# Kernel optimization log

Measured on AMD Instinct MI355X. Metric: run time of the kernel, lower is better.

Reference implementation:

```python
import jax, jax.numpy as jnp
import numpy as np

N_TOTAL = 524288  # total entity embeddings in flat ragged buffer
A = 262144        # number of actors
D = 256           # d_model
C = 32            # n_choice


def setup_inputs() -> dict:
    key = jax.random.key(0)
    k1, k2, k3, k4, k5 = jax.random.split(key, 5)
    x_data = jax.random.normal(k1, (N_TOTAL, D), dtype=jnp.float32)
    W = jax.random.normal(k2, (C, D), dtype=jnp.float32) * 0.01  # layer_init std=0.01
    b = jnp.zeros((C,), dtype=jnp.float32)
    actors = jax.random.randint(k3, (A,), 0, N_TOTAL, dtype=jnp.int64)
    mask = jax.random.randint(k4, (A, C), 0, 2, dtype=jnp.int32)
    mask = mask.at[:, 0].set(1)  # guarantee at least one valid choice per actor
    pa = jax.random.randint(k5, (A,), 0, C, dtype=jnp.int64)
    # prev_actions must be valid under the mask (as a real rollout would be)
    valid = jnp.take_along_axis(mask, pa[:, None], axis=1).squeeze(-1)
    prev_actions = jnp.where(valid != 0, pa, 0)
    return {"x_data": x_data, "W": W, "b": b, "actors": actors,
            "mask": mask, "prev_actions": prev_actions}


def reference(x_data, W, b, actors, mask, prev_actions):
    # gather actor embeddings: [A, D]
    actor_embeds = x_data[actors]
    # linear projection: [A, C]
    logits = jnp.einsum('ad,cd->ac', actor_embeds, W) + b
    # masked fill with -inf where mask == 0
    logits = jnp.where(mask == 0, -jnp.inf, logits)
    # Categorical: normalized logits = log_softmax
    logp = jax.nn.log_softmax(logits, axis=-1)
    p = jnp.exp(logp)
    action = prev_actions  # prev_actions provided -> no sampling
    logprob = jnp.take_along_axis(logp, action[:, None], axis=1).squeeze(-1)
    # entropy: -sum p*logp over valid entries (0*(-inf) -> 0)
    entropy = -jnp.sum(jnp.where(mask != 0, p * logp, 0.0), axis=-1)
    return action, logprob, entropy, logp
```

## Files before the change

### kernel.cpp

```cpp
#include <hip/hip_runtime.h>
#include <math.h>


constexpr int A_TOTAL = 262144;
constexpr int DMODEL  = 256;
constexpr int NCHOICE = 32;
constexpr int BATCH   = 32;
constexpr int PADC    = 36;

#define MASK_NEG 1.0e30f

#define DPP_SUM_STEP(x, ctrl)                                              \
    (x) += __int_as_float(__builtin_amdgcn_update_dpp(                     \
        0, __float_as_int(x), (ctrl), 0xf, 0xf, true))
#define DPP_MAX_STEP(x, ctrl)                                              \
    (x) = fmaxf((x), __int_as_float(__builtin_amdgcn_update_dpp(           \
        0, __float_as_int(x), (ctrl), 0xf, 0xf, true)))

#define DPP_REDUCE_DG(x)                                                   \
    do { DPP_SUM_STEP(x, 0xB1); DPP_SUM_STEP(x, 0x4E);                     \
         DPP_SUM_STEP(x, 0x128); DPP_SUM_STEP(x, 0x124); } while (0)

#define DPP_RED8_SUM(x)                                                    \
    do { DPP_SUM_STEP(x, 0xB1); DPP_SUM_STEP(x, 0x4E);                     \
         DPP_SUM_STEP(x, 0x141); } while (0)
#define DPP_RED8_MAX(x)                                                    \
    do { DPP_MAX_STEP(x, 0xB1); DPP_MAX_STEP(x, 0x4E);                     \
         DPP_MAX_STEP(x, 0x141); } while (0)

__global__ __launch_bounds__(256, 2)
void cat_action_head(const float* __restrict__ x_data,
                     const float* __restrict__ W,
                     const float* __restrict__ bvec,
                     const int*   __restrict__ actors,
                     const int*   __restrict__ mask,
                     const int*   __restrict__ prev_actions,
                     float* __restrict__ out)
{
    const int t  = threadIdx.x;
    const int wv = t >> 6;
    const int ln = t & 63;
    const int dg = ln & 15;
    const int cg = ln >> 4;

    float* out_action  = out;
    float* out_logprob = out + A_TOTAL;
    float* out_entropy = out + 2 * A_TOTAL;
    float* out_logp    = out + 3 * A_TOTAL;

    __shared__ float xs[BATCH][DMODEL];
    __shared__ float part[BATCH][PADC];

    const int abase = blockIdx.x * BATCH;

    const int aa  = t >> 3;
    const int q   = t & 7;
    const int aep = abase + aa;
    const int4   mv  = *reinterpret_cast<const int4*>(
                           &mask[(size_t)aep * NCHOICE + q * 4]);
    const float4 bq  = *reinterpret_cast<const float4*>(&bvec[q * 4]);
    const int    act = prev_actions[aep];

    {
        int acts[8];
#pragma unroll
        for (int j = 0; j < 8; ++j)
            acts[j] = actors[abase + wv * 8 + j];
#pragma unroll
        for (int j = 0; j < 8; ++j) {
            const float* src = x_data + (size_t)acts[j] * DMODEL + ln * 4;
            __builtin_amdgcn_global_load_lds(
                (const __attribute__((address_space(1))) void*)src,
                (__attribute__((address_space(3))) void*)&xs[wv * 8 + j][0],
                16, 0, 0);
        }
    }

    float4 Wf[8][4];
#pragma unroll
    for (int k = 0; k < 8; ++k) {
        const float* Wr = W + (size_t)(cg * 8 + k) * DMODEL + dg * 4;
#pragma unroll
        for (int j = 0; j < 4; ++j)
            Wf[k][j] = *reinterpret_cast<const float4*>(Wr + j * 64);
    }

    asm volatile("s_waitcnt vmcnt(0)" ::: "memory");

#pragma unroll 1
    for (int ii = 0; ii < 8; ++ii) {
        const int i = wv * 8 + ii;
        const float* xrow = &xs[i][dg * 4];
        float4 xv[4];
#pragma unroll
        for (int j = 0; j < 4; ++j)
            xv[j] = *reinterpret_cast<const float4*>(xrow + j * 64);

        float acc[8] = {0.f, 0.f, 0.f, 0.f, 0.f, 0.f, 0.f, 0.f};
#pragma unroll
        for (int j = 0; j < 4; ++j) {
#pragma unroll
            for (int k = 0; k < 8; ++k) {
                acc[k] = fmaf(xv[j].x, Wf[k][j].x, acc[k]);
                acc[k] = fmaf(xv[j].y, Wf[k][j].y, acc[k]);
                acc[k] = fmaf(xv[j].z, Wf[k][j].z, acc[k]);
                acc[k] = fmaf(xv[j].w, Wf[k][j].w, acc[k]);
            }
        }
#pragma unroll
        for (int k = 0; k < 8; ++k) DPP_REDUCE_DG(acc[k]);

        if (dg == 0) {
            float4 v0; v0.x = acc[0]; v0.y = acc[1]; v0.z = acc[2]; v0.w = acc[3];
            float4 v1; v1.x = acc[4]; v1.y = acc[5]; v1.z = acc[6]; v1.w = acc[7];
            *reinterpret_cast<float4*>(&part[i][cg * 8])     = v0;
            *reinterpret_cast<float4*>(&part[i][cg * 8 + 4]) = v1;
        }
    }

    {
        const float4 pv = *reinterpret_cast<const float4*>(&part[aa][q * 4]);

        const float lg0 = mv.x ? pv.x + bq.x : -MASK_NEG;
        const float lg1 = mv.y ? pv.y + bq.y : -MASK_NEG;
        const float lg2 = mv.z ? pv.z + bq.z : -MASK_NEG;
        const float lg3 = mv.w ? pv.w + bq.w : -MASK_NEG;

        float mx = fmaxf(fmaxf(lg0, lg1), fmaxf(lg2, lg3));
        DPP_RED8_MAX(mx);

        const float e0 = expf(lg0 - mx);
        const float e1 = expf(lg1 - mx);
        const float e2 = expf(lg2 - mx);
        const float e3 = expf(lg3 - mx);
        float se = (e0 + e1) + (e2 + e3);
        DPP_RED8_SUM(se);

        const float lse = mx + logf(se);
        const float rse = 1.0f / se;

        const float lp0 = lg0 - lse;
        const float lp1 = lg1 - lse;
        const float lp2 = lg2 - lse;
        const float lp3 = lg3 - lse;

        float4 lpv; lpv.x = lp0; lpv.y = lp1; lpv.z = lp2; lpv.w = lp3;
        *reinterpret_cast<float4*>(
            &out_logp[(size_t)aep * NCHOICE + q * 4]) = lpv;

        float ent = fmaf(e0, lp0, fmaf(e1, lp1, fmaf(e2, lp2, e3 * lp3)));
        DPP_RED8_SUM(ent);

        float sel = (act == q * 4 + 0) ? lp0 : 0.0f;
        sel = (act == q * 4 + 1) ? lp1 : sel;
        sel = (act == q * 4 + 2) ? lp2 : sel;
        sel = (act == q * 4 + 3) ? lp3 : sel;
        DPP_RED8_SUM(sel);

        if (q == 0) {
            out_logprob[aep] = sel;
            out_entropy[aep] = -ent * rse;
            out_action[aep]  = (float)act;
        }
    }
}

extern "C" void kernel_launch(void* const* d_in, const int* in_sizes, int n_in,
                              void* d_out, int out_size, void* d_ws, size_t ws_size,
                              hipStream_t stream)
{
    const float* x_data = (const float*)d_in[0];
    const float* W      = (const float*)d_in[1];
    const float* bvec   = (const float*)d_in[2];
    const int*   actors = (const int*)d_in[3];
    const int*   mask   = (const int*)d_in[4];
    const int*   prev   = (const int*)d_in[5];
    float*       o      = (float*)d_out;

    const int nblocks = A_TOTAL / BATCH;
    cat_action_head<<<nblocks, 256, 0, stream>>>(x_data, W, bvec, actors, mask,
                                                 prev, o);
}
```

Before: 107.1 us.

## Process 64 actors per block with double-buffered LDS gather pipeline

Each block now handles 64 actors, and each wave processes 16 of them in two chunks of 8. The gather into LDS for the second chunk is issued before computing the first, with a partial vmcnt wait so the gather overlaps the GEMV. Actor indices are loaded as int4 vectors, and LDS reads of the next row are software-prefetched during compute. In exchange, the W register load is amortized over twice as many actors, but there are half as many blocks and more LDS per block, which may reduce occupancy and latency hiding.

```diff
diff --git a/kernel.cpp b/kernel.cpp
--- a/kernel.cpp
+++ b/kernel.cpp
@@ -5,7 +5,7 @@
 constexpr int A_TOTAL = 262144;
 constexpr int DMODEL  = 256;
 constexpr int NCHOICE = 32;
-constexpr int BATCH   = 32;
+constexpr int APB     = 64;
 constexpr int PADC    = 36;
 
 #define MASK_NEG 1.0e30f
@@ -20,7 +20,6 @@
 #define DPP_REDUCE_DG(x)                                                   \
     do { DPP_SUM_STEP(x, 0xB1); DPP_SUM_STEP(x, 0x4E);                     \
          DPP_SUM_STEP(x, 0x128); DPP_SUM_STEP(x, 0x124); } while (0)
-
 #define DPP_RED8_SUM(x)                                                    \
     do { DPP_SUM_STEP(x, 0xB1); DPP_SUM_STEP(x, 0x4E);                     \
          DPP_SUM_STEP(x, 0x141); } while (0)
@@ -48,33 +47,49 @@
     float* out_entropy = out + 2 * A_TOTAL;
     float* out_logp    = out + 3 * A_TOTAL;
 
-    __shared__ float xs[BATCH][DMODEL];
-    __shared__ float part[BATCH][PADC];
-
-    const int abase = blockIdx.x * BATCH;
-
-    const int aa  = t >> 3;
-    const int q   = t & 7;
-    const int aep = abase + aa;
-    const int4   mv  = *reinterpret_cast<const int4*>(
-                           &mask[(size_t)aep * NCHOICE + q * 4]);
+    __shared__ float xs[4][2][8][DMODEL];
+    __shared__ float part[APB][PADC];
+
+    const int bbase = blockIdx.x * APB;
+    const int wb    = bbase + wv * 16;
+
+    const int q  = ln & 7;
+    const int p0 = wv * 16 + (ln >> 3);
+    const int p1 = p0 + 8;
+    const int a0 = bbase + p0;
+    const int a1 = bbase + p1;
+    const int4   mv0 = *reinterpret_cast<const int4*>(&mask[(size_t)a0 * NCHOICE + q * 4]);
+    const int4   mv1 = *reinterpret_cast<const int4*>(&mask[(size_t)a1 * NCHOICE + q * 4]);
     const float4 bq  = *reinterpret_cast<const float4*>(&bvec[q * 4]);
-    const int    act = prev_actions[aep];
-
+    const int    act0 = prev_actions[a0];
+    const int    act1 = prev_actions[a1];
+
+    int acts[16];
     {
-        int acts[8];
-#pragma unroll
-        for (int j = 0; j < 8; ++j)
-            acts[j] = actors[abase + wv * 8 + j];
-#pragma unroll
-        for (int j = 0; j < 8; ++j) {
-            const float* src = x_data + (size_t)acts[j] * DMODEL + ln * 4;
-            __builtin_amdgcn_global_load_lds(
-                (const __attribute__((address_space(1))) void*)src,
-                (__attribute__((address_space(3))) void*)&xs[wv * 8 + j][0],
-                16, 0, 0);
-        }
+        const int4 v0 = *reinterpret_cast<const int4*>(&actors[wb]);
+        const int4 v1 = *reinterpret_cast<const int4*>(&actors[wb + 4]);
+        const int4 v2 = *reinterpret_cast<const int4*>(&actors[wb + 8]);
+        const int4 v3 = *reinterpret_cast<const int4*>(&actors[wb + 12]);
+        acts[0]=v0.x; acts[1]=v0.y; acts[2]=v0.z; acts[3]=v0.w;
+        acts[4]=v1.x; acts[5]=v1.y; acts[6]=v1.z; acts[7]=v1.w;
+        acts[8]=v2.x; acts[9]=v2.y; acts[10]=v2.z; acts[11]=v2.w;
+        acts[12]=v3.x; acts[13]=v3.y; acts[14]=v3.z; acts[15]=v3.w;
     }
+
+#define STAGE(BUF, C)                                                       \
+    do {                                                                    \
+        _Pragma("unroll")                                                   \
+        for (int j = 0; j < 8; ++j) {                                       \
+            const float* src = x_data + (size_t)acts[(C) * 8 + j] * DMODEL  \
+                             + ln * 4;                                      \
+            __builtin_amdgcn_global_load_lds(                               \
+                (const __attribute__((address_space(1))) void*)src,         \
+                (__attribute__((address_space(3))) void*)&xs[wv][BUF][j][0],\
+                16, 0, 0);                                                  \
+        }                                                                   \
+    } while (0)
+
+    STAGE(0, 0);
 
     float4 Wf[8][4];
 #pragma unroll
@@ -85,84 +100,104 @@
             Wf[k][j] = *reinterpret_cast<const float4*>(Wr + j * 64);
     }
 
+    STAGE(1, 1);
+
+#define LDR(DST, BUF, II)                                                   \
+    do {                                                                    \
+        const float* xrow_ = &xs[wv][BUF][II][dg * 4];                      \
+        _Pragma("unroll")                                                   \
+        for (int j = 0; j < 4; ++j)                                         \
+            DST[j] = *reinterpret_cast<const float4*>(xrow_ + j * 64);      \
+    } while (0)
+
+#define COMPUTE(XV, C, II)                                                  \
+    do {                                                                    \
+        float acc[8] = {0.f,0.f,0.f,0.f,0.f,0.f,0.f,0.f};                   \
+        _Pragma("unroll")                                                   \
+        for (int j = 0; j < 4; ++j) {                                       \
+            _Pragma("unroll")                                               \
+            for (int k = 0; k < 8; ++k) {                                   \
+                acc[k] = fmaf(XV[j].x, Wf[k][j].x, acc[k]);                 \
+                acc[k] = fmaf(XV[j].y, Wf[k][j].y, acc[k]);                 \
+                acc[k] = fmaf(XV[j].z, Wf[k][j].z, acc[k]);                 \
+                acc[k] = fmaf(XV[j].w, Wf[k][j].w, acc[k]);                 \
+            }                                                               \
+        }                                                                   \
+        _Pragma("unroll")                                                   \
+        for (int k = 0; k < 8; ++k) DPP_REDUCE_DG(acc[k]);                  \
+        if (dg == 0) {                                                      \
+            const int p_ = wv * 16 + (C) * 8 + (II);                        \
+            float4 v0_; v0_.x=acc[0]; v0_.y=acc[1]; v0_.z=acc[2]; v0_.w=acc[3]; \
+            float4 v1_; v1_.x=acc[4]; v1_.y=acc[5]; v1_.z=acc[6]; v1_.w=acc[7]; \
+            *reinterpret_cast<float4*>(&part[p_][cg * 8])     = v0_;        \
+            *reinterpret_cast<float4*>(&part[p_][cg * 8 + 4]) = v1_;        \
+        }                                                                   \
+    } while (0)
+
+#define GEMV_CHUNK(C)                                                       \
+    do {                                                                    \
+        float4 xva[4], xvb[4];                                              \
+        LDR(xva, (C) & 1, 0);                                               \
+        _Pragma("unroll")                                                   \
+        for (int ii = 0; ii < 8; ii += 2) {                                 \
+            if (ii + 1 < 8) LDR(xvb, (C) & 1, ii + 1);                      \
+            COMPUTE(xva, C, ii);                                            \
+            if (ii + 2 < 8) LDR(xva, (C) & 1, ii + 2);                      \
+            COMPUTE(xvb, C, ii + 1);                                        \
+        }                                                                   \
+    } while (0)
+
+    asm volatile("s_waitcnt vmcnt(8)" ::: "memory");
+    GEMV_CHUNK(0);
     asm volatile("s_waitcnt vmcnt(0)" ::: "memory");
-
-#pragma unroll 1
-    for (int ii = 0; ii < 8; ++ii) {
-        const int i = wv * 8 + ii;
-        const float* xrow = &xs[i][dg * 4];
-        float4 xv[4];
-#pragma unroll
-        for (int j = 0; j < 4; ++j)
-            xv[j] = *reinterpret_cast<const float4*>(xrow + j * 64);
-
-        float acc[8] = {0.f, 0.f, 0.f, 0.f, 0.f, 0.f, 0.f, 0.f};
-#pragma unroll
-        for (int j = 0; j < 4; ++j) {
-#pragma unroll
-            for (int k = 0; k < 8; ++k) {
-                acc[k] = fmaf(xv[j].x, Wf[k][j].x, acc[k]);
-                acc[k] = fmaf(xv[j].y, Wf[k][j].y, acc[k]);
-                acc[k] = fmaf(xv[j].z, Wf[k][j].z, acc[k]);
-                acc[k] = fmaf(xv[j].w, Wf[k][j].w, acc[k]);
-            }
-        }
-#pragma unroll
-        for (int k = 0; k < 8; ++k) DPP_REDUCE_DG(acc[k]);
-
-        if (dg == 0) {
-            float4 v0; v0.x = acc[0]; v0.y = acc[1]; v0.z = acc[2]; v0.w = acc[3];
-            float4 v1; v1.x = acc[4]; v1.y = acc[5]; v1.z = acc[6]; v1.w = acc[7];
-            *reinterpret_cast<float4*>(&part[i][cg * 8])     = v0;
-            *reinterpret_cast<float4*>(&part[i][cg * 8 + 4]) = v1;
-        }
-    }
-
-    {
-        const float4 pv = *reinterpret_cast<const float4*>(&part[aa][q * 4]);
-
-        const float lg0 = mv.x ? pv.x + bq.x : -MASK_NEG;
-        const float lg1 = mv.y ? pv.y + bq.y : -MASK_NEG;
-        const float lg2 = mv.z ? pv.z + bq.z : -MASK_NEG;
-        const float lg3 = mv.w ? pv.w + bq.w : -MASK_NEG;
-
-        float mx = fmaxf(fmaxf(lg0, lg1), fmaxf(lg2, lg3));
-        DPP_RED8_MAX(mx);
-
-        const float e0 = expf(lg0 - mx);
-        const float e1 = expf(lg1 - mx);
-        const float e2 = expf(lg2 - mx);
-        const float e3 = expf(lg3 - mx);
-        float se = (e0 + e1) + (e2 + e3);
-        DPP_RED8_SUM(se);
-
-        const float lse = mx + logf(se);
-        const float rse = 1.0f / se;
-
-        const float lp0 = lg0 - lse;
-        const float lp1 = lg1 - lse;
-        const float lp2 = lg2 - lse;
-        const float lp3 = lg3 - lse;
-
-        float4 lpv; lpv.x = lp0; lpv.y = lp1; lpv.z = lp2; lpv.w = lp3;
-        *reinterpret_cast<float4*>(
-            &out_logp[(size_t)aep * NCHOICE + q * 4]) = lpv;
-
-        float ent = fmaf(e0, lp0, fmaf(e1, lp1, fmaf(e2, lp2, e3 * lp3)));
-        DPP_RED8_SUM(ent);
-
-        float sel = (act == q * 4 + 0) ? lp0 : 0.0f;
-        sel = (act == q * 4 + 1) ? lp1 : sel;
-        sel = (act == q * 4 + 2) ? lp2 : sel;
-        sel = (act == q * 4 + 3) ? lp3 : sel;
-        DPP_RED8_SUM(sel);
-
-        if (q == 0) {
-            out_logprob[aep] = sel;
-            out_entropy[aep] = -ent * rse;
-            out_action[aep]  = (float)act;
-        }
-    }
+    GEMV_CHUNK(1);
+
+#define EPILOGUE(PROW, AEP, MV, ACT)                                        \
+    do {                                                                    \
+        const float4 pv = *reinterpret_cast<const float4*>(&part[PROW][q * 4]); \
+        const float lg0 = (MV).x ? pv.x + bq.x : -MASK_NEG;                 \
+        const float lg1 = (MV).y ? pv.y + bq.y : -MASK_NEG;                 \
+        const float lg2 = (MV).z ? pv.z + bq.z : -MASK_NEG;                 \
+        const float lg3 = (MV).w ? pv.w + bq.w : -MASK_NEG;                 \
+        float mx = fmaxf(fmaxf(lg0, lg1), fmaxf(lg2, lg3));                 \
+        DPP_RED8_MAX(mx);                                                   \
+        const float e0 = expf(lg0 - mx);                                    \
+        const float e1 = expf(lg1 - mx);                                    \
+        const float e2 = expf(lg2 - mx);                                    \
+        const float e3 = expf(lg3 - mx);                                    \
+        float se = (e0 + e1) + (e2 + e3);                                   \
+        DPP_RED8_SUM(se);                                                   \
+        const float lse = mx + logf(se);                                    \
+        const float rse = 1.0f / se;                                        \
+        const float lp0 = lg0 - lse;                                        \
+        const float lp1 = lg1 - lse;                                        \
+        const float lp2 = lg2 - lse;                                        \
+        const float lp3 = lg3 - lse;                                        \
+        float4 lpv; lpv.x=lp0; lpv.y=lp1; lpv.z=lp2; lpv.w=lp3;             \
+        *reinterpret_cast<float4*>(                                         \
+            &out_logp[(size_t)(AEP) * NCHOICE + q * 4]) = lpv;              \
+        float ent = fmaf(e0, lp0, fmaf(e1, lp1, fmaf(e2, lp2, e3 * lp3)));  \
+        DPP_RED8_SUM(ent);                                                  \
+        float sel = ((ACT) == q * 4 + 0) ? lp0 : 0.0f;                      \
+        sel = ((ACT) == q * 4 + 1) ? lp1 : sel;                             \
+        sel = ((ACT) == q * 4 + 2) ? lp2 : sel;                             \
+        sel = ((ACT) == q * 4 + 3) ? lp3 : sel;                             \
+        DPP_RED8_SUM(sel);                                                  \
+        if (q == 0) {                                                       \
+            out_logprob[AEP] = sel;                                         \
+            out_entropy[AEP] = -ent * rse;                                  \
+            out_action[AEP]  = (float)(ACT);                                \
+        }                                                                   \
+    } while (0)
+
+    EPILOGUE(p0, a0, mv0, act0);
+    EPILOGUE(p1, a1, mv1, act1);
+
+#undef EPILOGUE
+#undef GEMV_CHUNK
+#undef COMPUTE
+#undef LDR
+#undef STAGE
 }
 
 extern "C" void kernel_launch(void* const* d_in, const int* in_sizes, int n_in,
@@ -177,7 +212,7 @@
     const int*   prev   = (const int*)d_in[5];
     float*       o      = (float*)d_out;
 
-    const int nblocks = A_TOTAL / BATCH;
+    const int nblocks = A_TOTAL / APB;
     cat_action_head<<<nblocks, 256, 0, stream>>>(x_data, W, bvec, actors, mask,
                                                  prev, o);
 }
```

Result: faster. 94.75 us (-11.5%).
